# Optimization experiments

Hardware: AMD Instinct MI355X
Metric: run time of the kernel (lower is better)

Reference implementation:

```python
import jax, jax.numpy as jnp
import numpy as np

CHEB_K = 3

def setup_inputs() -> dict:
    key = jax.random.key(0)
    ks = jax.random.split(key, 6)
    bs, node, in_dim, out_dim = 8, 1024, 64, 64
    d_e, t_d, embed_dim = 10, 6, 16
    return {
        "x": jax.random.normal(ks[0], (bs, node, in_dim), dtype=jnp.float32),
        "node_emb": jax.random.normal(ks[1], (node, d_e), dtype=jnp.float32),
        "t": jax.random.normal(ks[2], (bs, t_d), dtype=jnp.float32),
        "n_t": jax.random.normal(ks[3], (bs, t_d), dtype=jnp.float32),
        "p": jnp.zeros((1,), dtype=jnp.float32),
        "weights_pool": jax.random.normal(ks[4], (embed_dim, CHEB_K, in_dim, out_dim), dtype=jnp.float32),
        "bias_pool": jax.random.normal(ks[5], (embed_dim, out_dim), dtype=jnp.float32),
    }

def reference(x, node_emb, t, n_t, p, weights_pool, bias_pool):
    # x: [bs, node, in_dim]; node_emb: [node, d_e]; t, n_t: [bs, t_d]
    bs, node, _ = x.shape
    # static adjacency logits shared across batch: [node, node]
    a = node_emb @ node_emb.T
    # temporal scalar per batch: bmm of [bs,1,t_d] x [bs,t_d,1] -> [bs,1,1]
    a_t = jnp.einsum('bd,bd->b', n_t, t)[:, None, None]
    _a = a[None, :, :] + a_t                       # [bs, node, node]
    # period=False branch
    A = jax.nn.softmax(jax.nn.relu(_a), axis=2)    # [bs, node, node]
    # Chebyshev recursion: T0=I, T1=A, Tk = 2A@T_{k-1} - T_{k-2}
    I = jnp.broadcast_to(jnp.eye(node, dtype=x.dtype), (bs, node, node))
    supports = [I, A]
    for _ in range(2, CHEB_K):
        supports.append(jnp.matmul(2.0 * A, supports[-1]) - supports[-2])
    cheb = jnp.stack(supports, axis=1)             # [bs, k, node, node]
    # node+time embedding: [bs, node, d_e + t_d] = [bs, node, embed_dim]
    emb = jnp.concatenate(
        [jnp.broadcast_to(node_emb[None], (bs, node, node_emb.shape[1])),
         jnp.broadcast_to(n_t[:, None, :], (bs, node, n_t.shape[1]))], axis=-1)
    # graph conv: x_g[b,n,k,i] = sum_m cheb[b,k,n,m] x[b,m,i]
    x_g = jnp.einsum('bknm,bmc->bnkc', cheb, x)
    # fuse per-node weight generation into final contraction (same math as
    # weights = einsum('bnd,dkio->bnkio') followed by einsum('bnki,bnkio->bno'))
    out = jnp.einsum('bnki,bnd,dkio->bno', x_g, emb, weights_pool)
    bias = jnp.einsum('bnd,do->bno', emb, bias_pool)
    return out + bias
```

## Files before the change

kernel.cpp:

```cpp
#include <hip/hip_runtime.h>
#include <hip/hip_bf16.h>

#define NODE 1024
#define BS 8

struct alignas(8) bf4 { __hip_bfloat16 a, b, c, d; };
typedef short short8 __attribute__((ext_vector_type(8)));
typedef float f32x16 __attribute__((ext_vector_type(16)));

__device__ __forceinline__ short bf16bits(float f) {
    __hip_bfloat16 h = __float2bfloat16(f);
    return *reinterpret_cast<short*>(&h);
}
__device__ __forceinline__ float bitstofl(short s) {
    unsigned u = ((unsigned)(unsigned short)s) << 16;
    return __uint_as_float(u);
}


__global__ __launch_bounds__(512) void k_attn(const float* __restrict__ ne,
                                              const float* __restrict__ t,
                                              const float* __restrict__ nt,
                                              __hip_bfloat16* __restrict__ A16f) {
    __shared__ float nel[NODE * 11];
    __shared__ float ssum[8][32];
    int tid = threadIdx.x;
    int w = tid >> 6, lane = tid & 63;
    int l31 = lane & 31, hi = lane >> 5;
    int bidx = blockIdx.x;
    int b = bidx >> 5;
    int n = (bidx & 31) * 32 + l31;

    for (int i = tid; i < NODE * 10; i += 512) nel[(i / 10) * 11 + (i % 10)] = ne[i];

    float at = 0.f;
#pragma unroll
    for (int j = 0; j < 6; ++j) at += nt[b * 6 + j] * t[b * 6 + j];
    __syncthreads();

    float nr[10];
#pragma unroll
    for (int d = 0; d < 10; ++d) nr[d] = nel[n * 11 + d];

    int mbase = w * 128 + hi * 64;
    float z[64];
#pragma unroll
    for (int m = 0; m < 64; ++m) {
        const float* row = &nel[(mbase + m) * 11];
        float s = 0.f;
#pragma unroll
        for (int d = 0; d < 10; ++d) s += nr[d] * row[d];
        z[m] = s;
    }

    short8 u16[8];
    float s = 0.f;
#pragma unroll
    for (int c = 0; c < 8; ++c) {
        short8 pk;
#pragma unroll
        for (int j = 0; j < 8; ++j) {
            float u = __expf(fmaxf(z[c * 8 + j] + at, 0.f));
            s += u;
            pk[j] = bf16bits(u);
        }
        u16[c] = pk;
    }
    s += __shfl_xor(s, 32);
    if (hi == 0) ssum[w][l31] = s;
    __syncthreads();
    float tot = 0.f;
#pragma unroll
    for (int ww = 0; ww < 8; ++ww) tot += ssum[ww][l31];
    float inv = 1.f / tot;

    __hip_bfloat16* base = A16f + ((size_t)(bidx * 64 + w * 8 + hi * 4) * 2) * 256 + l31 * 8;
#pragma unroll
    for (int c = 0; c < 8; ++c) {
        short8 pk = u16[c];
        short8 o;
#pragma unroll
        for (int j = 0; j < 8; ++j) o[j] = bf16bits(bitstofl(pk[j]) * inv);
        *(short8*)(base + c * 256) = o;
    }
}

__global__ __launch_bounds__(256) void k_prepw(const float* __restrict__ x,
                                               const float* __restrict__ W,
                                               const float* __restrict__ bp,
                                               __hip_bfloat16* __restrict__ xTf,
                                               __hip_bfloat16* __restrict__ xgf,
                                               __hip_bfloat16* __restrict__ wtf) {
    int tid = threadIdx.x;
    if (blockIdx.x < 128) {
        __shared__ __hip_bfloat16 T[64][72];
        int b = blockIdx.x >> 4;
        int n0 = (blockIdx.x & 15) * 64;
#pragma unroll
        for (int it = 0; it < 2; ++it) {
            int i = it * 256 + tid;
            int l31 = i & 31, hi2 = (i >> 5) & 1, ks = (i >> 6) & 3, rt = i >> 8;
            int node = n0 + rt * 32 + l31;
            const float* src = x + ((size_t)b * 1024 + node) * 64 + ks * 16 + hi2 * 8;
            short8 o;
#pragma unroll
            for (int j = 0; j < 8; ++j) o[j] = bf16bits(src[j]);
            size_t rtg = (size_t)b * 32 + (n0 >> 5) + rt;
            *(short8*)(xgf + (rtg * 13 + ks) * 512 + hi2 * 256 + l31 * 8) = o;
#pragma unroll
            for (int j = 0; j < 8; ++j) {
                __hip_bfloat16 h;
                *reinterpret_cast<short*>(&h) = o[j];
                T[ks * 16 + hi2 * 8 + j][rt * 32 + l31] = h;
            }
        }
        for (int i = tid; i < 1024; i += 256) {
            int rt = i >> 9, e = i & 511;
            size_t rtg = (size_t)b * 32 + (n0 >> 5) + rt;
            float val = ((e & 7) == 0 && e < 256) ? 1.0f : 0.0f;
            xgf[(rtg * 13 + 12) * 512 + e] = __float2bfloat16(val);
        }
        __syncthreads();
#pragma unroll
        for (int fh = 0; fh < 2; ++fh) {
            int f = fh * 32 + (tid & 31);
            int m8 = tid >> 5;
            int m = n0 + m8 * 8;
            short8 o;
#pragma unroll
            for (int j = 0; j < 8; ++j) {
                __hip_bfloat16 h = T[f][m8 * 8 + j];
                o[j] = *reinterpret_cast<short*>(&h);
            }
            size_t addr = (((size_t)(b * 2 + fh) * 64 + (m >> 4)) * 2 + ((m >> 3) & 1)) * 256 + (f & 31) * 8;
            *(short8*)(xTf + addr) = o;
        }
    } else {
        int d = blockIdx.x - 128;
        const float* Wd = W + (size_t)d * 192 * 64;
        for (int i = tid; i < 1664; i += 256) {
            int l31 = i & 31, hi2 = (i >> 5) & 1;
            int ks = (i >> 6) % 13, oh = (i >> 6) / 13;
            int o = oh * 32 + l31;
            short8 v;
#pragma unroll
            for (int j = 0; j < 8; ++j) {
                int k = ks * 16 + hi2 * 8 + j;
                float f = (k < 192) ? Wd[(size_t)k * 64 + o]
                                    : ((k == 192) ? bp[d * 64 + o] : 0.0f);
                v[j] = bf16bits(f);
            }
            size_t addr = ((((size_t)d * 2 + oh) * 13 + ks) * 2 + hi2) * 256 + l31 * 8;
            *(short8*)(wtf + addr) = v;
        }
    }
}

#define LOADG(slot, g) do {                                                   \
    as[slot][0] = *(const short8*)(pa + ((g) * 4 + 0) * 512);                 \
    as[slot][1] = *(const short8*)(pa + ((g) * 4 + 1) * 512);                 \
    as[slot][2] = *(const short8*)(pa + ((g) * 4 + 2) * 512);                 \
    as[slot][3] = *(const short8*)(pa + ((g) * 4 + 3) * 512);                 \
    bs[slot][0] = *(const short8*)(pb + ((g) * 4 + 0) * 512);                 \
    bs[slot][1] = *(const short8*)(pb + ((g) * 4 + 1) * 512);                 \
    bs[slot][2] = *(const short8*)(pb + ((g) * 4 + 2) * 512);                 \
    bs[slot][3] = *(const short8*)(pb + ((g) * 4 + 3) * 512);                 \
} while (0)

template<bool FIRST>
__global__ __launch_bounds__(256) void k_spmm_mfma(const __hip_bfloat16* __restrict__ A16f,
                                                   const __hip_bfloat16* __restrict__ srcTf,
                                                   const float* __restrict__ xres,
                                                   __hip_bfloat16* __restrict__ xgf,
                                                   __hip_bfloat16* __restrict__ y1Tf) {
    __shared__ float P[2][32][67];
    int b = blockIdx.x >> 5;
    int ntile = blockIdx.x & 31;
    int n0 = ntile << 5;
    int tid = threadIdx.x;
    int wv = tid >> 6, lane = tid & 63;
    int fh = wv & 1, kh = wv >> 1;
    int l31 = lane & 31, hi = lane >> 5;

    const __hip_bfloat16* pa = srcTf + (((size_t)(b * 2 + fh) * 64 + kh * 32) * 2 + hi) * 256 + l31 * 8;
    const __hip_bfloat16* pb = A16f + (((size_t)(b * 32 + ntile) * 64 + kh * 32) * 2 + hi) * 256 + l31 * 8;

    f32x16 acc0, acc1;
#pragma unroll
    for (int i = 0; i < 16; ++i) { acc0[i] = 0.f; acc1[i] = 0.f; }

    short8 as[3][4], bs[3][4];
    LOADG(0, 0);
    LOADG(1, 1);
#pragma unroll
    for (int g = 0; g < 8; ++g) {
        if (g + 2 < 8) { LOADG((g + 2) % 3, g + 2); }
        int cu = g % 3;
        acc0 = __builtin_amdgcn_mfma_f32_32x32x16_bf16(as[cu][0], bs[cu][0], acc0, 0, 0, 0);
        acc1 = __builtin_amdgcn_mfma_f32_32x32x16_bf16(as[cu][1], bs[cu][1], acc1, 0, 0, 0);
        acc0 = __builtin_amdgcn_mfma_f32_32x32x16_bf16(as[cu][2], bs[cu][2], acc0, 0, 0, 0);
        acc1 = __builtin_amdgcn_mfma_f32_32x32x16_bf16(as[cu][3], bs[cu][3], acc1, 0, 0, 0);
    }
#pragma unroll
    for (int i = 0; i < 16; ++i) acc0[i] += acc1[i];

    if (kh == 1) {
#pragma unroll
        for (int r = 0; r < 16; ++r) {
            int f = hi * 4 + (r >> 2) * 8 + (r & 3);
            P[fh][l31][f] = acc0[r];
        }
    }
    __syncthreads();
    if (kh == 0) {
#pragma unroll
        for (int r = 0; r < 16; ++r) {
            int f = hi * 4 + (r >> 2) * 8 + (r & 3);
            acc0[r] += P[fh][l31][f];
        }

        int node = n0 + l31;
        size_t row = (size_t)(b << 10) + node;
        size_t rtg = (size_t)b * 32 + ntile;
#pragma unroll
        for (int rg = 0; rg < 4; ++rg) {
            int fb = fh * 32 + hi * 4 + rg * 8;
            float vx = acc0[rg * 4], vy = acc0[rg * 4 + 1];
            float vz = acc0[rg * 4 + 2], vw = acc0[rg * 4 + 3];
            if (!FIRST) {
                float4 xv = *(const float4*)(xres + row * 64 + fb);
                vx = 2.f * vx - xv.x; vy = 2.f * vy - xv.y;
                vz = 2.f * vz - xv.z; vw = 2.f * vw - xv.w;
            }
            bf4 o;
            o.a = __float2bfloat16(vx); o.b = __float2bfloat16(vy);
            o.c = __float2bfloat16(vz); o.d = __float2bfloat16(vw);
            int kstep = (FIRST ? 4 : 8) + fh * 2 + (rg >> 1);
            int hi2 = rg & 1;
            *(bf4*)(xgf + (rtg * 13 + kstep) * 512 + hi2 * 256 + l31 * 8 + hi * 4) = o;
        }
        if (FIRST) {
#pragma unroll
            for (int r = 0; r < 16; ++r) {
                int f = fh * 32 + hi * 4 + (r >> 2) * 8 + (r & 3);
                size_t addr = (((size_t)(b * 2 + fh) * 64 + ((n0 + l31) >> 4)) * 2 + ((l31 >> 3) & 1)) * 256
                              + (f & 31) * 8 + (l31 & 7);
                __hip_bfloat16 h = __float2bfloat16(acc0[r]);
                y1Tf[addr] = h;
            }
        }
    }
}

__global__ __launch_bounds__(512) void k_fuse(const __hip_bfloat16* __restrict__ xgf,
                                              const __hip_bfloat16* __restrict__ wtf,
                                              const float* __restrict__ ne,
                                              const float* __restrict__ nt,
                                              float* __restrict__ out) {
    __shared__ float P[8][32][67];
    int rt = blockIdx.x;
    int m0 = rt * 32;
    int tid = threadIdx.x;
    int w = tid >> 6;
    int lane = tid & 63;
    int l31 = lane & 31, hi = lane >> 5;
    int b = m0 >> 10;
    int n = (m0 & 1023) + l31;

    int d0 = 2 * w, d1 = 2 * w + 1;
    float e0 = (d0 < 10) ? ne[n * 10 + d0] : nt[b * 6 + (d0 - 10)];
    float e1 = (d1 < 10) ? ne[n * 10 + d1] : nt[b * 6 + (d1 - 10)];

    short8 xf[13];
    const __hip_bfloat16* px = xgf + (size_t)rt * 6656 + hi * 256 + l31 * 8;
#pragma unroll
    for (int k = 0; k < 13; ++k) xf[k] = *(const short8*)(px + k * 512);

    f32x16 z00, z01, z10, z11;
#pragma unroll
    for (int i = 0; i < 16; ++i) { z00[i] = 0.f; z01[i] = 0.f; z10[i] = 0.f; z11[i] = 0.f; }

    const __hip_bfloat16* pw0 = wtf + (size_t)d0 * 13312 + hi * 256 + l31 * 8;
#pragma unroll
    for (int k = 0; k < 13; ++k) {
        short8 a00 = *(const short8*)(pw0 + k * 512);
        short8 a01 = *(const short8*)(pw0 + 6656 + k * 512);
        short8 a10 = *(const short8*)(pw0 + 13312 + k * 512);
        short8 a11 = *(const short8*)(pw0 + 13312 + 6656 + k * 512);
        z00 = __builtin_amdgcn_mfma_f32_32x32x16_bf16(a00, xf[k], z00, 0, 0, 0);
        z01 = __builtin_amdgcn_mfma_f32_32x32x16_bf16(a01, xf[k], z01, 0, 0, 0);
        z10 = __builtin_amdgcn_mfma_f32_32x32x16_bf16(a10, xf[k], z10, 0, 0, 0);
        z11 = __builtin_amdgcn_mfma_f32_32x32x16_bf16(a11, xf[k], z11, 0, 0, 0);
    }

#pragma unroll
    for (int r = 0; r < 16; ++r) {
        int o = (r & 3) + 8 * (r >> 2) + 4 * hi;
        P[w][l31][o]      = e0 * z00[r] + e1 * z10[r];
        P[w][l31][o + 32] = e0 * z01[r] + e1 * z11[r];
    }
    __syncthreads();

    int m = tid >> 4, o0 = (tid & 15) * 4;
    float s0 = 0.f, s1 = 0.f, s2 = 0.f, s3 = 0.f;
#pragma unroll
    for (int ww = 0; ww < 8; ++ww) {
        s0 += P[ww][m][o0];
        s1 += P[ww][m][o0 + 1];
        s2 += P[ww][m][o0 + 2];
        s3 += P[ww][m][o0 + 3];
    }
    *(float4*)(out + (size_t)(m0 + m) * 64 + o0) = make_float4(s0, s1, s2, s3);
}

extern "C" void kernel_launch(void* const* d_in, const int* in_sizes, int n_in,
                              void* d_out, int out_size, void* d_ws, size_t ws_size,
                              hipStream_t stream) {
    const float* x  = (const float*)d_in[0];
    const float* ne = (const float*)d_in[1];
    const float* t  = (const float*)d_in[2];
    const float* nt = (const float*)d_in[3];
    const float* W  = (const float*)d_in[5];
    const float* bp = (const float*)d_in[6];
    float* out = (float*)d_out;

    __hip_bfloat16* wsb = (__hip_bfloat16*)d_ws;
    __hip_bfloat16* A16f = wsb;
    __hip_bfloat16* xTf  = wsb + 8388608;
    __hip_bfloat16* y1Tf = wsb + 8912896;
    __hip_bfloat16* xgf  = wsb + 9437184;
    __hip_bfloat16* wtf  = wsb + 11141120;

    k_attn<<<BS * 32, 512, 0, stream>>>(ne, t, nt, A16f);
    k_prepw<<<144, 256, 0, stream>>>(x, W, bp, xTf, xgf, wtf);
    k_spmm_mfma<true ><<<BS * 32, 256, 0, stream>>>(A16f, xTf,  x, xgf, y1Tf);
    k_spmm_mfma<false><<<BS * 32, 256, 0, stream>>>(A16f, y1Tf, x, xgf, nullptr);
    k_fuse<<<BS * (NODE / 32), 512, 0, stream>>>(xgf, wtf, ne, nt, out);
}
```

Measured before the change: 123.4 us.

## Fuse all stages into one persistent kernel with grid barriers and LDS-resident attention

The five launches (attention softmax, input/weight prep, two Chebyshev SpMM passes and the final fused contraction) become one persistent kernel of 256 blocks, synchronised by two atomic grid barriers. Each block computes its own 32-row slice of the softmax adjacency directly into LDS in MFMA fragment layout and reuses it for both SpMM passes. This removes the large bf16 adjacency round trip through global memory and the per-launch overheads. In exchange it relies on all 256 blocks, each using about 136KB of LDS, being co-resident. It also adds spin-wait barrier cost and a memset for the barrier counters.

Measured after the change: 155.1 us. 25.7% more time.

```diff
diff --git a/kernel.cpp b/kernel.cpp
--- a/kernel.cpp
+++ b/kernel.cpp
@@ -3,6 +3,7 @@
 
 #define NODE 1024
 #define BS 8
+#define NBLK 256
 
 struct alignas(8) bf4 { __hip_bfloat16 a, b, c, d; };
 typedef short short8 __attribute__((ext_vector_type(8)));
@@ -12,221 +13,66 @@
     __hip_bfloat16 h = __float2bfloat16(f);
     return *reinterpret_cast<short*>(&h);
 }
-__device__ __forceinline__ float bitstofl(short s) {
-    unsigned u = ((unsigned)(unsigned short)s) << 16;
-    return __uint_as_float(u);
-}
-
-
-__global__ __launch_bounds__(512) void k_attn(const float* __restrict__ ne,
-                                              const float* __restrict__ t,
-                                              const float* __restrict__ nt,
-                                              __hip_bfloat16* __restrict__ A16f) {
-    __shared__ float nel[NODE * 11];
-    __shared__ float ssum[8][32];
-    int tid = threadIdx.x;
-    int w = tid >> 6, lane = tid & 63;
-    int l31 = lane & 31, hi = lane >> 5;
-    int bidx = blockIdx.x;
-    int b = bidx >> 5;
-    int n = (bidx & 31) * 32 + l31;
-
-    for (int i = tid; i < NODE * 10; i += 512) nel[(i / 10) * 11 + (i % 10)] = ne[i];
-
-    float at = 0.f;
-#pragma unroll
-    for (int j = 0; j < 6; ++j) at += nt[b * 6 + j] * t[b * 6 + j];
-    __syncthreads();
-
-    float nr[10];
-#pragma unroll
-    for (int d = 0; d < 10; ++d) nr[d] = nel[n * 11 + d];
-
-    int mbase = w * 128 + hi * 64;
-    float z[64];
-#pragma unroll
-    for (int m = 0; m < 64; ++m) {
-        const float* row = &nel[(mbase + m) * 11];
-        float s = 0.f;
-#pragma unroll
-        for (int d = 0; d < 10; ++d) s += nr[d] * row[d];
-        z[m] = s;
-    }
-
-    short8 u16[8];
-    float s = 0.f;
-#pragma unroll
-    for (int c = 0; c < 8; ++c) {
-        short8 pk;
-#pragma unroll
-        for (int j = 0; j < 8; ++j) {
-            float u = __expf(fmaxf(z[c * 8 + j] + at, 0.f));
-            s += u;
-            pk[j] = bf16bits(u);
-        }
-        u16[c] = pk;
-    }
-    s += __shfl_xor(s, 32);
-    if (hi == 0) ssum[w][l31] = s;
-    __syncthreads();
-    float tot = 0.f;
-#pragma unroll
-    for (int ww = 0; ww < 8; ++ww) tot += ssum[ww][l31];
-    float inv = 1.f / tot;
-
-    __hip_bfloat16* base = A16f + ((size_t)(bidx * 64 + w * 8 + hi * 4) * 2) * 256 + l31 * 8;
-#pragma unroll
-    for (int c = 0; c < 8; ++c) {
-        short8 pk = u16[c];
-        short8 o;
-#pragma unroll
-        for (int j = 0; j < 8; ++j) o[j] = bf16bits(bitstofl(pk[j]) * inv);
-        *(short8*)(base + c * 256) = o;
-    }
-}
-
-__global__ __launch_bounds__(256) void k_prepw(const float* __restrict__ x,
-                                               const float* __restrict__ W,
-                                               const float* __restrict__ bp,
-                                               __hip_bfloat16* __restrict__ xTf,
-                                               __hip_bfloat16* __restrict__ xgf,
-                                               __hip_bfloat16* __restrict__ wtf) {
-    int tid = threadIdx.x;
-    if (blockIdx.x < 128) {
-        __shared__ __hip_bfloat16 T[64][72];
-        int b = blockIdx.x >> 4;
-        int n0 = (blockIdx.x & 15) * 64;
-#pragma unroll
-        for (int it = 0; it < 2; ++it) {
-            int i = it * 256 + tid;
-            int l31 = i & 31, hi2 = (i >> 5) & 1, ks = (i >> 6) & 3, rt = i >> 8;
-            int node = n0 + rt * 32 + l31;
-            const float* src = x + ((size_t)b * 1024 + node) * 64 + ks * 16 + hi2 * 8;
-            short8 o;
-#pragma unroll
-            for (int j = 0; j < 8; ++j) o[j] = bf16bits(src[j]);
-            size_t rtg = (size_t)b * 32 + (n0 >> 5) + rt;
-            *(short8*)(xgf + (rtg * 13 + ks) * 512 + hi2 * 256 + l31 * 8) = o;
-#pragma unroll
-            for (int j = 0; j < 8; ++j) {
-                __hip_bfloat16 h;
-                *reinterpret_cast<short*>(&h) = o[j];
-                T[ks * 16 + hi2 * 8 + j][rt * 32 + l31] = h;
-            }
-        }
-        for (int i = tid; i < 1024; i += 256) {
-            int rt = i >> 9, e = i & 511;
-            size_t rtg = (size_t)b * 32 + (n0 >> 5) + rt;
-            float val = ((e & 7) == 0 && e < 256) ? 1.0f : 0.0f;
-            xgf[(rtg * 13 + 12) * 512 + e] = __float2bfloat16(val);
-        }
-        __syncthreads();
-#pragma unroll
-        for (int fh = 0; fh < 2; ++fh) {
-            int f = fh * 32 + (tid & 31);
-            int m8 = tid >> 5;
-            int m = n0 + m8 * 8;
-            short8 o;
-#pragma unroll
-            for (int j = 0; j < 8; ++j) {
-                __hip_bfloat16 h = T[f][m8 * 8 + j];
-                o[j] = *reinterpret_cast<short*>(&h);
-            }
-            size_t addr = (((size_t)(b * 2 + fh) * 64 + (m >> 4)) * 2 + ((m >> 3) & 1)) * 256 + (f & 31) * 8;
-            *(short8*)(xTf + addr) = o;
-        }
-    } else {
-        int d = blockIdx.x - 128;
-        const float* Wd = W + (size_t)d * 192 * 64;
-        for (int i = tid; i < 1664; i += 256) {
-            int l31 = i & 31, hi2 = (i >> 5) & 1;
-            int ks = (i >> 6) % 13, oh = (i >> 6) / 13;
-            int o = oh * 32 + l31;
-            short8 v;
-#pragma unroll
-            for (int j = 0; j < 8; ++j) {
-                int k = ks * 16 + hi2 * 8 + j;
-                float f = (k < 192) ? Wd[(size_t)k * 64 + o]
-                                    : ((k == 192) ? bp[d * 64 + o] : 0.0f);
-                v[j] = bf16bits(f);
-            }
-            size_t addr = ((((size_t)d * 2 + oh) * 13 + ks) * 2 + hi2) * 256 + l31 * 8;
-            *(short8*)(wtf + addr) = v;
-        }
-    }
-}
-
-#define LOADG(slot, g) do {                                                   \
-    as[slot][0] = *(const short8*)(pa + ((g) * 4 + 0) * 512);                 \
-    as[slot][1] = *(const short8*)(pa + ((g) * 4 + 1) * 512);                 \
-    as[slot][2] = *(const short8*)(pa + ((g) * 4 + 2) * 512);                 \
-    as[slot][3] = *(const short8*)(pa + ((g) * 4 + 3) * 512);                 \
-    bs[slot][0] = *(const short8*)(pb + ((g) * 4 + 0) * 512);                 \
-    bs[slot][1] = *(const short8*)(pb + ((g) * 4 + 1) * 512);                 \
-    bs[slot][2] = *(const short8*)(pb + ((g) * 4 + 2) * 512);                 \
-    bs[slot][3] = *(const short8*)(pb + ((g) * 4 + 3) * 512);                 \
-} while (0)
+
+
+__device__ __forceinline__ void gridbar(unsigned* c) {
+    __syncthreads();
+    if (threadIdx.x == 0) {
+        __threadfence();
+        __hip_atomic_fetch_add(c, 1u, __ATOMIC_ACQ_REL, __HIP_MEMORY_SCOPE_AGENT);
+        while (__hip_atomic_load(c, __ATOMIC_ACQUIRE, __HIP_MEMORY_SCOPE_AGENT) < NBLK)
+            __builtin_amdgcn_s_sleep(2);
+    }
+    __syncthreads();
+}
 
 template<bool FIRST>
-__global__ __launch_bounds__(256) void k_spmm_mfma(const __hip_bfloat16* __restrict__ A16f,
-                                                   const __hip_bfloat16* __restrict__ srcTf,
-                                                   const float* __restrict__ xres,
-                                                   __hip_bfloat16* __restrict__ xgf,
-                                                   __hip_bfloat16* __restrict__ y1Tf) {
-    __shared__ float P[2][32][67];
-    int b = blockIdx.x >> 5;
-    int ntile = blockIdx.x & 31;
-    int n0 = ntile << 5;
-    int tid = threadIdx.x;
-    int wv = tid >> 6, lane = tid & 63;
-    int fh = wv & 1, kh = wv >> 1;
-    int l31 = lane & 31, hi = lane >> 5;
-
-    const __hip_bfloat16* pa = srcTf + (((size_t)(b * 2 + fh) * 64 + kh * 32) * 2 + hi) * 256 + l31 * 8;
-    const __hip_bfloat16* pb = A16f + (((size_t)(b * 32 + ntile) * 64 + kh * 32) * 2 + hi) * 256 + l31 * 8;
-
-    f32x16 acc0, acc1;
-#pragma unroll
-    for (int i = 0; i < 16; ++i) { acc0[i] = 0.f; acc1[i] = 0.f; }
-
-    short8 as[3][4], bs[3][4];
-    LOADG(0, 0);
-    LOADG(1, 1);
-#pragma unroll
-    for (int g = 0; g < 8; ++g) {
-        if (g + 2 < 8) { LOADG((g + 2) % 3, g + 2); }
-        int cu = g % 3;
-        acc0 = __builtin_amdgcn_mfma_f32_32x32x16_bf16(as[cu][0], bs[cu][0], acc0, 0, 0, 0);
-        acc1 = __builtin_amdgcn_mfma_f32_32x32x16_bf16(as[cu][1], bs[cu][1], acc1, 0, 0, 0);
-        acc0 = __builtin_amdgcn_mfma_f32_32x32x16_bf16(as[cu][2], bs[cu][2], acc0, 0, 0, 0);
-        acc1 = __builtin_amdgcn_mfma_f32_32x32x16_bf16(as[cu][3], bs[cu][3], acc1, 0, 0, 0);
-    }
-#pragma unroll
-    for (int i = 0; i < 16; ++i) acc0[i] += acc1[i];
-
-    if (kh == 1) {
+__device__ __forceinline__ void spmm_phase(const __hip_bfloat16* A_lds,
+                                           float (*P)[2][32][33],
+                                           const __hip_bfloat16* __restrict__ srcTf,
+                                           const float* __restrict__ xres,
+                                           __hip_bfloat16* __restrict__ xgf,
+                                           __hip_bfloat16* __restrict__ y1Tf,
+                                           int b, int ntile, int w, int l31, int hi) {
+    int fh = w & 1, kq = w >> 1;
+    const __hip_bfloat16* pa = srcTf + (((size_t)(b * 2 + fh) * 64 + kq * 16) * 2 + hi) * 256 + l31 * 8;
+    const __hip_bfloat16* pb = A_lds + ((size_t)(kq * 16) * 2 + hi) * 256 + l31 * 8;
+
+    f32x16 a0, a1;
+#pragma unroll
+    for (int i = 0; i < 16; ++i) { a0[i] = 0.f; a1[i] = 0.f; }
+#pragma unroll
+    for (int gi = 0; gi < 16; gi += 2) {
+        short8 av0 = *(const short8*)(pa + (size_t)gi * 512);
+        short8 bv0 = *(const short8*)(pb + (size_t)gi * 512);
+        short8 av1 = *(const short8*)(pa + (size_t)gi * 512 + 512);
+        short8 bv1 = *(const short8*)(pb + (size_t)gi * 512 + 512);
+        a0 = __builtin_amdgcn_mfma_f32_32x32x16_bf16(av0, bv0, a0, 0, 0, 0);
+        a1 = __builtin_amdgcn_mfma_f32_32x32x16_bf16(av1, bv1, a1, 0, 0, 0);
+    }
+#pragma unroll
+    for (int i = 0; i < 16; ++i) a0[i] += a1[i];
+
+    if (kq != 0) {
+#pragma unroll
+        for (int r = 0; r < 16; ++r)
+            P[kq - 1][fh][l31][hi * 4 + (r >> 2) * 8 + (r & 3)] = a0[r];
+    }
+    __syncthreads();
+    if (kq == 0) {
 #pragma unroll
         for (int r = 0; r < 16; ++r) {
             int f = hi * 4 + (r >> 2) * 8 + (r & 3);
-            P[fh][l31][f] = acc0[r];
-        }
-    }
-    __syncthreads();
-    if (kh == 0) {
-#pragma unroll
-        for (int r = 0; r < 16; ++r) {
-            int f = hi * 4 + (r >> 2) * 8 + (r & 3);
-            acc0[r] += P[fh][l31][f];
-        }
-
-        int node = n0 + l31;
-        size_t row = (size_t)(b << 10) + node;
+            a0[r] += P[0][fh][l31][f] + P[1][fh][l31][f] + P[2][fh][l31][f];
+        }
         size_t rtg = (size_t)b * 32 + ntile;
+        int node = ntile * 32 + l31;
+        size_t row = (size_t)b * 1024 + node;
 #pragma unroll
         for (int rg = 0; rg < 4; ++rg) {
             int fb = fh * 32 + hi * 4 + rg * 8;
-            float vx = acc0[rg * 4], vy = acc0[rg * 4 + 1];
-            float vz = acc0[rg * 4 + 2], vw = acc0[rg * 4 + 3];
+            float vx = a0[rg * 4], vy = a0[rg * 4 + 1];
+            float vz = a0[rg * 4 + 2], vw = a0[rg * 4 + 3];
             if (!FIRST) {
                 float4 xv = *(const float4*)(xres + row * 64 + fb);
                 vx = 2.f * vx - xv.x; vy = 2.f * vy - xv.y;
@@ -236,81 +82,213 @@
             o.a = __float2bfloat16(vx); o.b = __float2bfloat16(vy);
             o.c = __float2bfloat16(vz); o.d = __float2bfloat16(vw);
             int kstep = (FIRST ? 4 : 8) + fh * 2 + (rg >> 1);
-            int hi2 = rg & 1;
-            *(bf4*)(xgf + (rtg * 13 + kstep) * 512 + hi2 * 256 + l31 * 8 + hi * 4) = o;
+            *(bf4*)(xgf + (rtg * 13 + kstep) * 512 + (rg & 1) * 256 + l31 * 8 + hi * 4) = o;
         }
         if (FIRST) {
 #pragma unroll
             for (int r = 0; r < 16; ++r) {
                 int f = fh * 32 + hi * 4 + (r >> 2) * 8 + (r & 3);
-                size_t addr = (((size_t)(b * 2 + fh) * 64 + ((n0 + l31) >> 4)) * 2 + ((l31 >> 3) & 1)) * 256
+                size_t addr = (((size_t)(b * 2 + fh) * 64 + (node >> 4)) * 2 + ((l31 >> 3) & 1)) * 256
                               + (f & 31) * 8 + (l31 & 7);
-                __hip_bfloat16 h = __float2bfloat16(acc0[r]);
-                y1Tf[addr] = h;
+                y1Tf[addr] = __float2bfloat16(a0[r]);
             }
         }
     }
 }
 
-__global__ __launch_bounds__(512) void k_fuse(const __hip_bfloat16* __restrict__ xgf,
-                                              const __hip_bfloat16* __restrict__ wtf,
-                                              const float* __restrict__ ne,
-                                              const float* __restrict__ nt,
-                                              float* __restrict__ out) {
-    __shared__ float P[8][32][67];
-    int rt = blockIdx.x;
-    int m0 = rt * 32;
+__global__ __launch_bounds__(512) void k_all(const float* __restrict__ x,
+                                             const float* __restrict__ ne,
+                                             const float* __restrict__ t,
+                                             const float* __restrict__ nt,
+                                             const float* __restrict__ W,
+                                             const float* __restrict__ bp,
+                                             __hip_bfloat16* __restrict__ xTf,
+                                             __hip_bfloat16* __restrict__ y1Tf,
+                                             __hip_bfloat16* __restrict__ xgf,
+                                             __hip_bfloat16* __restrict__ wtf,
+                                             unsigned* __restrict__ bar,
+                                             float* __restrict__ out) {
+    __shared__ __align__(16) char bufA[110592];
+    __shared__ __align__(16) char bufB[25344];
+    __hip_bfloat16* A_lds = (__hip_bfloat16*)bufA;
+    float* nel = (float*)(bufA + 65536);
+    typedef __hip_bfloat16 row72[72];
+    row72* T = (row72*)bufB;
+    typedef float p_t[2][32][33];
+    p_t* P = (p_t*)bufB;
+    typedef float pf_t[32][67];
+    pf_t* PF = (pf_t*)bufA;
+
+    int bidx = blockIdx.x;
     int tid = threadIdx.x;
-    int w = tid >> 6;
-    int lane = tid & 63;
+    int w = tid >> 6, lane = tid & 63;
     int l31 = lane & 31, hi = lane >> 5;
-    int b = m0 >> 10;
-    int n = (m0 & 1023) + l31;
-
-    int d0 = 2 * w, d1 = 2 * w + 1;
-    float e0 = (d0 < 10) ? ne[n * 10 + d0] : nt[b * 6 + (d0 - 10)];
-    float e1 = (d1 < 10) ? ne[n * 10 + d1] : nt[b * 6 + (d1 - 10)];
-
-    short8 xf[13];
-    const __hip_bfloat16* px = xgf + (size_t)rt * 6656 + hi * 256 + l31 * 8;
-#pragma unroll
-    for (int k = 0; k < 13; ++k) xf[k] = *(const short8*)(px + k * 512);
-
-    f32x16 z00, z01, z10, z11;
-#pragma unroll
-    for (int i = 0; i < 16; ++i) { z00[i] = 0.f; z01[i] = 0.f; z10[i] = 0.f; z11[i] = 0.f; }
-
-    const __hip_bfloat16* pw0 = wtf + (size_t)d0 * 13312 + hi * 256 + l31 * 8;
-#pragma unroll
-    for (int k = 0; k < 13; ++k) {
-        short8 a00 = *(const short8*)(pw0 + k * 512);
-        short8 a01 = *(const short8*)(pw0 + 6656 + k * 512);
-        short8 a10 = *(const short8*)(pw0 + 13312 + k * 512);
-        short8 a11 = *(const short8*)(pw0 + 13312 + 6656 + k * 512);
-        z00 = __builtin_amdgcn_mfma_f32_32x32x16_bf16(a00, xf[k], z00, 0, 0, 0);
-        z01 = __builtin_amdgcn_mfma_f32_32x32x16_bf16(a01, xf[k], z01, 0, 0, 0);
-        z10 = __builtin_amdgcn_mfma_f32_32x32x16_bf16(a10, xf[k], z10, 0, 0, 0);
-        z11 = __builtin_amdgcn_mfma_f32_32x32x16_bf16(a11, xf[k], z11, 0, 0, 0);
-    }
-
-#pragma unroll
-    for (int r = 0; r < 16; ++r) {
-        int o = (r & 3) + 8 * (r >> 2) + 4 * hi;
-        P[w][l31][o]      = e0 * z00[r] + e1 * z10[r];
-        P[w][l31][o + 32] = e0 * z01[r] + e1 * z11[r];
-    }
-    __syncthreads();
-
-    int m = tid >> 4, o0 = (tid & 15) * 4;
-    float s0 = 0.f, s1 = 0.f, s2 = 0.f, s3 = 0.f;
-#pragma unroll
-    for (int ww = 0; ww < 8; ++ww) {
-        s0 += P[ww][m][o0];
-        s1 += P[ww][m][o0 + 1];
-        s2 += P[ww][m][o0 + 2];
-        s3 += P[ww][m][o0 + 3];
-    }
-    *(float4*)(out + (size_t)(m0 + m) * 64 + o0) = make_float4(s0, s1, s2, s3);
+    int b = bidx >> 5, ntile = bidx & 31;
+
+    for (int i = tid; i < NODE * 10; i += 512) nel[(i / 10) * 11 + (i % 10)] = ne[i];
+    float at = 0.f;
+#pragma unroll
+    for (int j = 0; j < 6; ++j) at += nt[b * 6 + j] * t[b * 6 + j];
+    __syncthreads();
+
+    float nr[4][10];
+#pragma unroll
+    for (int rr = 0; rr < 4; ++rr) {
+        int n = ntile * 32 + w * 4 + rr;
+#pragma unroll
+        for (int d = 0; d < 10; ++d) nr[rr][d] = nel[n * 11 + d];
+    }
+    float z[4][16];
+#pragma unroll
+    for (int j = 0; j < 16; ++j) {
+        int m = lane + (j << 6);
+        float mr[10];
+#pragma unroll
+        for (int d = 0; d < 10; ++d) mr[d] = nel[m * 11 + d];
+#pragma unroll
+        for (int rr = 0; rr < 4; ++rr) {
+            float s = 0.f;
+#pragma unroll
+            for (int d = 0; d < 10; ++d) s += nr[rr][d] * mr[d];
+            z[rr][j] = s;
+        }
+    }
+
+    if (bidx < 128) {
+        int pb = bidx >> 4, pn0 = (bidx & 15) * 64;
+        {
+            int i = tid;
+            int il = i & 31, ih = (i >> 5) & 1, iks = (i >> 6) & 3, irt = i >> 8;
+            int node = pn0 + irt * 32 + il;
+            const float* src = x + ((size_t)pb * 1024 + node) * 64 + iks * 16 + ih * 8;
+            short8 o;
+#pragma unroll
+            for (int j = 0; j < 8; ++j) o[j] = bf16bits(src[j]);
+            size_t rtg = (size_t)pb * 32 + (pn0 >> 5) + irt;
+            *(short8*)(xgf + (rtg * 13 + iks) * 512 + ih * 256 + il * 8) = o;
+#pragma unroll
+            for (int j = 0; j < 8; ++j) {
+                __hip_bfloat16 h;
+                *reinterpret_cast<short*>(&h) = o[j];
+                T[iks * 16 + ih * 8 + j][irt * 32 + il] = h;
+            }
+        }
+        for (int q = tid; q < 1024; q += 512) {
+            int qrt = q >> 9, e = q & 511;
+            size_t rtg = (size_t)pb * 32 + (pn0 >> 5) + qrt;
+            xgf[(rtg * 13 + 12) * 512 + e] = __float2bfloat16(((e & 7) == 0 && e < 256) ? 1.0f : 0.0f);
+        }
+    } else if (bidx < 144) {
+        int d = bidx - 128;
+        const float* Wd = W + (size_t)d * 192 * 64;
+        for (int i = tid; i < 1664; i += 512) {
+            int il = i & 31, ih = (i >> 5) & 1;
+            int ks = (i >> 6) % 13, oh = (i >> 6) / 13;
+            int o = oh * 32 + il;
+            short8 v;
+#pragma unroll
+            for (int j = 0; j < 8; ++j) {
+                int k = ks * 16 + ih * 8 + j;
+                float f = (k < 192) ? Wd[(size_t)k * 64 + o]
+                                    : ((k == 192) ? bp[d * 64 + o] : 0.0f);
+                v[j] = bf16bits(f);
+            }
+            *(short8*)(wtf + ((((size_t)d * 2 + oh) * 13 + ks) * 2 + ih) * 256 + il * 8) = v;
+        }
+    }
+    __syncthreads();
+
+#pragma unroll
+    for (int rr = 0; rr < 4; ++rr) {
+        float s = 0.f;
+#pragma unroll
+        for (int j = 0; j < 16; ++j) {
+            float u = __expf(fmaxf(z[rr][j] + at, 0.f));
+            z[rr][j] = u;
+            s += u;
+        }
+#pragma unroll
+        for (int off = 32; off > 0; off >>= 1) s += __shfl_xor(s, off);
+        float inv = 1.f / s;
+        int nloc = w * 4 + rr;
+#pragma unroll
+        for (int j = 0; j < 16; ++j) {
+            int idx = (((lane >> 4) + 4 * j) * 2 + ((lane >> 3) & 1)) * 256 + nloc * 8 + (lane & 7);
+            A_lds[idx] = __float2bfloat16(z[rr][j] * inv);
+        }
+    }
+    if (bidx < 128) {
+        int pb = bidx >> 4, pn0 = (bidx & 15) * 64;
+        int fh2 = tid >> 8, inner = tid & 255;
+        int f = fh2 * 32 + (inner & 31), m8 = inner >> 5;
+        int m = pn0 + m8 * 8;
+        short8 o;
+#pragma unroll
+        for (int j = 0; j < 8; ++j) {
+            __hip_bfloat16 h = T[f][m8 * 8 + j];
+            o[j] = *reinterpret_cast<short*>(&h);
+        }
+        *(short8*)(xTf + (((size_t)(pb * 2 + fh2) * 64 + (m >> 4)) * 2 + ((m >> 3) & 1)) * 256 + (f & 31) * 8) = o;
+    }
+
+    gridbar(&bar[0]);
+
+    spmm_phase<true>(A_lds, P, xTf, x, xgf, y1Tf, b, ntile, w, l31, hi);
+
+    gridbar(&bar[1]);
+
+    spmm_phase<false>(A_lds, P, y1Tf, x, xgf, y1Tf, b, ntile, w, l31, hi);
+
+    __syncthreads();
+
+    {
+        int rt = bidx;
+        int m0 = rt * 32;
+        int n = ntile * 32 + l31;
+        int d0 = 2 * w, d1 = 2 * w + 1;
+        float e0 = (d0 < 10) ? ne[n * 10 + d0] : nt[b * 6 + (d0 - 10)];
+        float e1 = (d1 < 10) ? ne[n * 10 + d1] : nt[b * 6 + (d1 - 10)];
+
+        short8 xf[13];
+        const __hip_bfloat16* px = xgf + (size_t)rt * 6656 + hi * 256 + l31 * 8;
+#pragma unroll
+        for (int k = 0; k < 13; ++k) xf[k] = *(const short8*)(px + k * 512);
+
+        f32x16 z00, z01, z10, z11;
+#pragma unroll
+        for (int i = 0; i < 16; ++i) { z00[i] = 0.f; z01[i] = 0.f; z10[i] = 0.f; z11[i] = 0.f; }
+
+        const __hip_bfloat16* pw0 = wtf + (size_t)d0 * 13312 + hi * 256 + l31 * 8;
+#pragma unroll
+        for (int k = 0; k < 13; ++k) {
+            short8 a00 = *(const short8*)(pw0 + k * 512);
+            short8 a01 = *(const short8*)(pw0 + 6656 + k * 512);
+            short8 a10 = *(const short8*)(pw0 + 13312 + k * 512);
+            short8 a11 = *(const short8*)(pw0 + 13312 + 6656 + k * 512);
+            z00 = __builtin_amdgcn_mfma_f32_32x32x16_bf16(a00, xf[k], z00, 0, 0, 0);
+            z01 = __builtin_amdgcn_mfma_f32_32x32x16_bf16(a01, xf[k], z01, 0, 0, 0);
+            z10 = __builtin_amdgcn_mfma_f32_32x32x16_bf16(a10, xf[k], z10, 0, 0, 0);
+            z11 = __builtin_amdgcn_mfma_f32_32x32x16_bf16(a11, xf[k], z11, 0, 0, 0);
+        }
+#pragma unroll
+        for (int r = 0; r < 16; ++r) {
+            int o = (r & 3) + 8 * (r >> 2) + 4 * hi;
+            PF[w][l31][o]      = e0 * z00[r] + e1 * z10[r];
+            PF[w][l31][o + 32] = e0 * z01[r] + e1 * z11[r];
+        }
+        __syncthreads();
+
+        int m = tid >> 4, o0 = (tid & 15) * 4;
+        float s0 = 0.f, s1 = 0.f, s2 = 0.f, s3 = 0.f;
+#pragma unroll
+        for (int ww = 0; ww < 8; ++ww) {
+            s0 += PF[ww][m][o0];
+            s1 += PF[ww][m][o0 + 1];
+            s2 += PF[ww][m][o0 + 2];
+            s3 += PF[ww][m][o0 + 3];
+        }
+        *(float4*)(out + (size_t)(m0 + m) * 64 + o0) = make_float4(s0, s1, s2, s3);
+    }
 }
 
 extern "C" void kernel_launch(void* const* d_in, const int* in_sizes, int n_in,
@@ -325,15 +303,12 @@
     float* out = (float*)d_out;
 
     __hip_bfloat16* wsb = (__hip_bfloat16*)d_ws;
-    __hip_bfloat16* A16f = wsb;
-    __hip_bfloat16* xTf  = wsb + 8388608;
-    __hip_bfloat16* y1Tf = wsb + 8912896;
-    __hip_bfloat16* xgf  = wsb + 9437184;
-    __hip_bfloat16* wtf  = wsb + 11141120;
-
-    k_attn<<<BS * 32, 512, 0, stream>>>(ne, t, nt, A16f);
-    k_prepw<<<144, 256, 0, stream>>>(x, W, bp, xTf, xgf, wtf);
-    k_spmm_mfma<true ><<<BS * 32, 256, 0, stream>>>(A16f, xTf,  x, xgf, y1Tf);
-    k_spmm_mfma<false><<<BS * 32, 256, 0, stream>>>(A16f, y1Tf, x, xgf, nullptr);
-    k_fuse<<<BS * (NODE / 32), 512, 0, stream>>>(xgf, wtf, ne, nt, out);
-}
+    __hip_bfloat16* xTf  = wsb;
+    __hip_bfloat16* y1Tf = wsb + 524288;
+    __hip_bfloat16* xgf  = wsb + 1048576;
+    __hip_bfloat16* wtf  = wsb + 2752512;
+    unsigned* bar = (unsigned*)((char*)d_ws + (8u << 20));
+
+    hipMemsetAsync(bar, 0, 64, stream);
+    k_all<<<NBLK, 512, 0, stream>>>(x, ne, t, nt, W, bp, xTf, y1Tf, xgf, wtf, bar, out);
+}
```
